# Kernel tuning notes

Hardware: AMD Instinct MI355X
Metric: run time of the kernel (lower is better)

## Reference

```python
import jax, jax.numpy as jnp
import numpy as np

DEV_VDW, VDW_N, MAXV, MINV, DM_MIN = 0.2, 6.0, 0.0356, 0.0178, 0.5


def setup_inputs() -> dict:
    key = jax.random.key(0)
    ks = iter(jax.random.split(key, 64))
    B, N1, N2, D, L = 8, 128, 256, 128, 3
    f = jnp.float32
    nrm = lambda shape, s=0.05: jax.random.normal(next(ks), shape, f) * s
    ligand_h = jax.random.normal(next(ks), (B, N1, 54), f)
    target_h = jax.random.normal(next(ks), (B, N2, 54), f)
    def adj(n):
        a = (jax.random.uniform(next(ks), (B, n, n)) < 0.08).astype(f)
        a = jnp.maximum(a, jnp.swapaxes(a, 1, 2))
        return jnp.maximum(a, jnp.eye(n, dtype=f))
    ligand_adj = adj(N1)
    target_adj = adj(N2)
    interaction_indice = jax.random.uniform(next(ks), (B, 3, N1, N2), f)
    ligand_pos = jax.random.normal(next(ks), (B, N1, 3), f) * 2.0
    target_pos = jax.random.normal(next(ks), (B, N2, 3), f) * 4.0
    rotor = jax.random.uniform(next(ks), (B,), f) * 10.0
    ligand_vdw_radii = 1.2 + 0.8 * jax.random.uniform(next(ks), (B, N1), f)
    target_vdw_radii = 1.2 + 0.8 * jax.random.uniform(next(ks), (B, N2), f)
    return dict(
        ligand_h=ligand_h, ligand_adj=ligand_adj, target_h=target_h, target_adj=target_adj,
        interaction_indice=interaction_indice, ligand_pos=ligand_pos, target_pos=target_pos,
        rotor=rotor, ligand_vdw_radii=ligand_vdw_radii, target_vdw_radii=target_vdw_radii,
        ligand_valid=jnp.ones((B, N1), f), target_valid=jnp.ones((B, N2), f),
        ligand_non_metal=jnp.ones((B, N1), f), target_non_metal=jnp.ones((B, N2), f),
        emb_w=nrm((54, D)),
        gat_w=nrm((L, D, D)), gat_b=jnp.zeros((L, D), f), gat_att=nrm((L, D, D)),
        gat_gate_w=nrm((L, 2 * D, 1)), gat_gate_b=jnp.zeros((L, 1), f),
        int_wt_w=nrm((L, D, D)), int_wt_b=jnp.zeros((L, D), f),
        int_mt_w=nrm((L, D, D)), int_mt_b=jnp.zeros((L, D), f),
        gru_w_ih=nrm((L, 3 * D, D)), gru_w_hh=nrm((L, 3 * D, D)),
        gru_b_ih=jnp.zeros((L, 3 * D), f), gru_b_hh=jnp.zeros((L, 3 * D), f),
        A_w1=nrm((2 * D, D)), A_b1=jnp.zeros((D,), f), A_w2=nrm((D, 1)), A_b2=jnp.zeros((1,), f),
        B_w1=nrm((2 * D, D)), B_b1=jnp.zeros((D,), f), B_w2=nrm((D, 1)), B_b2=jnp.zeros((1,), f),
        hbond_coeff=jnp.array([1.0], f), hydrophobic_coeff=jnp.array([0.5], f),
        rotor_coeff=jnp.array([0.5], f),
    )


def reference(ligand_h, ligand_adj, target_h, target_adj, interaction_indice, ligand_pos,
              target_pos, rotor, ligand_vdw_radii, target_vdw_radii, ligand_valid,
              target_valid, ligand_non_metal, target_non_metal, emb_w, gat_w, gat_b,
              gat_att, gat_gate_w, gat_gate_b, int_wt_w, int_wt_b, int_mt_w, int_mt_b,
              gru_w_ih, gru_w_hh, gru_b_ih, gru_b_hh, A_w1, A_b1, A_w2, A_b2, B_w1, B_b1,
              B_w2, B_b2, hbond_coeff, hydrophobic_coeff, rotor_coeff):
    B, D, L = ligand_h.shape[0], emb_w.shape[1], gat_w.shape[0]

    def dist(lpos):
        diff = lpos[:, :, None, :] - target_pos[:, None, :, :]
        dm = jnp.sqrt((diff * diff).sum(-1) + 1e-10)
        return jnp.where(dm < DM_MIN, 1e10, dm)

    dm = dist(ligand_pos)

    def gat(x, adj, i):
        nt = x @ gat_w[i] + gat_b[i]                                   # [B,N,D]
        ea = jnp.einsum('bjl,bkl->bjk', nt @ gat_att[i], nt)
        ea = ea + jnp.swapaxes(ea, 1, 2)
        aw = jax.nn.softmax(jnp.where(adj > 1e-6, ea, -9e15), axis=-1) * adj
        out = jax.nn.relu(jnp.einsum('bij,bjd->bid', aw, nt))
        gate = jax.nn.sigmoid(jnp.concatenate([x, out], -1) @ gat_gate_w[i] + gat_gate_b[i])
        return gate * x + (1.0 - gate) * out

    lh = ligand_h @ emb_w
    th = target_h @ emb_w
    for i in range(L):
        lh = gat(lh, ligand_adj, i)
        th = gat(th, target_adj, i)

    adj12 = jax.lax.stop_gradient(dm)
    adj12 = jnp.where(adj12 > 5.0, 0.0, adj12)
    adj12 = jnp.where(adj12 > 1e-3, 1.0, 0.0)
    adj21 = jnp.swapaxes(adj12, 1, 2)

    def inter(a1, a2, ev, i):
        t1 = a1 @ int_wt_w[i] + int_wt_b[i]
        m2 = a2 @ int_mt_w[i] + int_mt_b[i]                            # [B,N2,D]
        t2 = (m2[:, None, :, :] * ev[..., None]).max(axis=2)           # [B,N1,D]
        msg = jax.nn.relu(t1 + t2)
        gi = msg @ gru_w_ih[i].T + gru_b_ih[i]
        gh = a1 @ gru_w_hh[i].T + gru_b_hh[i]
        i_r, i_z, i_n = jnp.split(gi, 3, -1)
        h_r, h_z, h_n = jnp.split(gh, 3, -1)
        r = jax.nn.sigmoid(i_r + h_r)
        z = jax.nn.sigmoid(i_z + h_z)
        n = jnp.tanh(i_n + r * h_n)
        return (1.0 - z) * n + z * a1

    for i in range(L):
        lh, th = inter(lh, th, adj12, i), inter(th, lh, adj21, i)

    N1, N2 = lh.shape[1], th.shape[1]
    h_cat = jnp.concatenate([
        jnp.broadcast_to(lh[:, :, None, :], (B, N1, N2, D)),
        jnp.broadcast_to(th[:, None, :, :], (B, N1, N2, D))], -1)      # [B,N1,N2,2D]

    A_raw = jax.nn.sigmoid(jax.nn.relu(h_cat @ A_w1 + A_b1) @ A_w2 + A_b2)[..., 0]
    B_raw = jnp.tanh(jax.nn.relu(h_cat @ B_w1 + B_b1) @ B_w2 + B_b2)[..., 0] * DEV_VDW
    dm0 = ligand_vdw_radii[:, :, None] + target_vdw_radii[:, None, :] + B_raw
    valid_pair = ligand_non_metal[:, :, None] * target_non_metal[:, None, :]
    A_vdw = A_raw * (MAXV - MINV) + MINV

    def energies_of(dm):
        dm0c = jnp.where(dm0 < 1e-4, 1.0, dm0)
        r6 = (dm0c / dm) ** VDW_N
        evdw = A_vdw * (jnp.minimum(r6 * r6 - 2.0 * r6, 100.0) * valid_pair)
        vdw_val = evdw.sum((1, 2))[:, None]
        dmd = dm - dm0
        def hb(Aind):
            r = jnp.clip(dmd * Aind / -0.7, 0.0, 1.0) * -(hbond_coeff[0] * hbond_coeff[0])
            return r.sum((1, 2))[:, None]
        hbond = hb(interaction_indice[:, 0])
        metal = hb(interaction_indice[:, 1])
        hp = jnp.clip((-dmd + 1.5) * interaction_indice[:, 2], 0.0, 1.0)
        hp = hp * -(hydrophobic_coeff[0] * hydrophobic_coeff[0])
        e = jnp.concatenate([vdw_val, hbond, metal, hp.sum((1, 2))[:, None]], -1)
        return e / (1.0 + rotor_coeff[0] * rotor_coeff[0] * rotor[:, None])

    energies = energies_of(dm)
    esum = lambda p: energies_of(dist(p)).sum()
    g = jax.grad(esum)(ligand_pos)
    der1 = (g.sum(1) ** 2).mean()
    der2 = -jax.grad(lambda p: jax.grad(esum)(p).sum())(ligand_pos).sum((1, 2)).mean()
    return energies, der1, der2
```

## Files before the change

### kernel.cpp

```cpp
#include <hip/hip_runtime.h>
#include <math.h>

#define BB 8
#define N1C 128
#define N2C 256
#define DC 128
#define NHC 54
#define ROWS_L 1024
#define ROWS_T 2048
#define ROWS_ALL 3072

__device__ __forceinline__ float wredSum(float v) {
#pragma unroll
  for (int o = 32; o > 0; o >>= 1) v += __shfl_down(v, o);
  return v;
}
__device__ float blockSum(float v) {
  __shared__ float red[9];
  v = wredSum(v);
  int lane = threadIdx.x & 63, wid = threadIdx.x >> 6;
  __syncthreads();
  if (lane == 0) red[wid] = v;
  __syncthreads();
  if (threadIdx.x == 0) {
    float s = 0.f;
    int nw = (blockDim.x + 63) >> 6;
    for (int i = 0; i < nw; ++i) s += red[i];
    red[8] = s;
  }
  __syncthreads();
  return red[8];
}

__global__ __launch_bounds__(256) void k_prep(
    const float* __restrict__ LP, const float* __restrict__ TP,
    float* __restrict__ AD, const float* __restrict__ LH,
    const float* __restrict__ TH, const float* __restrict__ EW,
    float* __restrict__ H0, const float* __restrict__ GWp,
    const float* __restrict__ GBp, const float* __restrict__ ATT,
    float* __restrict__ WA, float* __restrict__ bA,
    const float* __restrict__ IH, const float* __restrict__ HH,
    float* __restrict__ GIHT, float* __restrict__ GHHT) {
  int bid = blockIdx.x, tid = threadIdx.x;
  if (bid < 1024) {
    long idx = (long)bid * 256 + tid;
    int j = idx & (N2C - 1);
    long t = idx >> 8;
    int i = (int)(t & (N1C - 1));
    int b = (int)(t >> 7);
    float dx = LP[((long)b * N1C + i) * 3 + 0] - TP[((long)b * N2C + j) * 3 + 0];
    float dy = LP[((long)b * N1C + i) * 3 + 1] - TP[((long)b * N2C + j) * 3 + 1];
    float dz = LP[((long)b * N1C + i) * 3 + 2] - TP[((long)b * N2C + j) * 3 + 2];
    float d = sqrtf(dx * dx + dy * dy + dz * dz + 1e-10f);
    if (d < 0.5f) d = 1e10f;
    AD[idx] = (d <= 5.0f && d > 1e-3f) ? 1.f : 0.f;
  } else if (bid < 1024 + 384) {
    int r0 = (bid - 1024) * 8;
    __shared__ float xs[8][NHC];
    for (int t = tid; t < 8 * NHC; t += 256) {
      int rr = r0 + t / NHC, c = t % NHC;
      xs[t / NHC][c] = (rr < ROWS_L) ? LH[(long)rr * NHC + c]
                                     : TH[(long)(rr - ROWS_L) * NHC + c];
    }
    __syncthreads();
    int d = tid & 127, rb = (tid >> 7) * 4;
    float a[4] = {0.f, 0.f, 0.f, 0.f};
#pragma unroll 6
    for (int k = 0; k < NHC; ++k) {
      float wv = EW[(long)k * DC + d];
#pragma unroll
      for (int r = 0; r < 4; ++r) a[r] += xs[rb + r][k] * wv;
    }
#pragma unroll
    for (int r = 0; r < 4; ++r) H0[(long)(r0 + rb + r) * DC + d] = a[r];
  } else if (bid < 1024 + 384 + 99) {
    int q = bid - 1408;
    int l = q / 33, bx = q % 33;
    const float* Wl = GWp + (long)l * DC * DC;
    const float* Al = ATT + (long)l * DC * DC;
    if (bx == 32) {
      if (tid < 128) {
        float acc = 0.f;
#pragma unroll 8
        for (int m = 0; m < DC; ++m)
          acc += GBp[l * DC + m] * Al[(long)m * DC + tid];
        bA[l * DC + tid] = acc;
      }
    } else {
      __shared__ float xs2[4][DC];
      int r0 = bx * 4;
      for (int t = tid; t < 4 * DC; t += 256)
        xs2[t >> 7][t & 127] = Wl[(long)r0 * DC + t];
      __syncthreads();
      if (tid < 128) {
        int d = tid;
        float a0 = 0.f, a1 = 0.f, a2 = 0.f, a3 = 0.f;
#pragma unroll 8
        for (int m = 0; m < DC; ++m) {
          float av = Al[(long)m * DC + d];
          a0 += xs2[0][m] * av;
          a1 += xs2[1][m] * av;
          a2 += xs2[2][m] * av;
          a3 += xs2[3][m] * av;
        }
        float* out = WA + (long)l * DC * DC + (long)r0 * DC + d;
        out[0] = a0;
        out[DC] = a1;
        out[2 * DC] = a2;
        out[3 * DC] = a3;
      }
    }
  } else {
    long idx = (long)(bid - 1507) * 256 + tid;
    if (idx < 6L * 49152) {
      int a = (int)(idx / 49152);
      int rem = (int)(idx % 49152);
      int l = a >> 1, whh = a & 1;
      int c = rem / 384, rr = rem % 384;
      const float* src = (whh ? HH : IH) + (long)l * 49152;
      float* dst = (whh ? GHHT : GIHT) + (long)l * 49152;
      dst[(long)c * 384 + rr] = src[(long)rr * 128 + c];
    }
  }
}

__global__ __launch_bounds__(256) void k_lin2h(
    const float* __restrict__ X, const float* __restrict__ W1,
    const float* __restrict__ b1, const float* __restrict__ W2,
    const float* __restrict__ b2, float* __restrict__ Y1,
    float* __restrict__ Y2) {
  int r0 = blockIdx.x * 4;
  __shared__ float xs_t[DC][4];
  int tid = threadIdx.x;
  for (int t = tid; t < 4 * DC; t += 256) {
    int r = t >> 7, c = t & 127;
    xs_t[c][r] = X[(long)(r0 + r) * DC + c];
  }
  __syncthreads();
  int h = tid >> 7, d = tid & 127;
  const float* W = h ? W2 : W1;
  const float* bp = h ? b2 : b1;
  float* Y = h ? Y2 : Y1;
  float a0 = 0.f, a1 = 0.f, a2 = 0.f, a3 = 0.f;
#pragma unroll 8
  for (int k = 0; k < DC; ++k) {
    float4 xv = *(const float4*)&xs_t[k][0];
    float wv = W[(long)k * DC + d];
    a0 = fmaf(xv.x, wv, a0);
    a1 = fmaf(xv.y, wv, a1);
    a2 = fmaf(xv.z, wv, a2);
    a3 = fmaf(xv.w, wv, a3);
  }
  float bv = bp ? bp[d] : 0.f;
  Y[(long)(r0 + 0) * DC + d] = a0 + bv;
  Y[(long)(r0 + 1) * DC + d] = a1 + bv;
  Y[(long)(r0 + 2) * DC + d] = a2 + bv;
  Y[(long)(r0 + 3) * DC + d] = a3 + bv;
}

__global__ __launch_bounds__(256) void k_featall(
    const float* __restrict__ X, const float* __restrict__ Aw1,
    const float* __restrict__ Ab1, const float* __restrict__ Bw1,
    const float* __restrict__ Bb1, float* __restrict__ UA,
    float* __restrict__ UB, float* __restrict__ VAT,
    float* __restrict__ VBT) {
  int bid = blockIdx.x;
  bool lig = bid < 256;
  int r0 = lig ? bid * 4 : ROWS_L + (bid - 256) * 4;
  __shared__ float xs_t[DC][4];
  int tid = threadIdx.x;
  for (int t = tid; t < 4 * DC; t += 256) {
    int r = t >> 7, c = t & 127;
    xs_t[c][r] = X[(long)(r0 + r) * DC + c];
  }
  __syncthreads();
  int h = tid >> 7, d = tid & 127;
  const float* W = (h ? Bw1 : Aw1) + (lig ? 0 : DC * DC);
  float a0 = 0.f, a1 = 0.f, a2 = 0.f, a3 = 0.f;
#pragma unroll 8
  for (int k = 0; k < DC; ++k) {
    float4 xv = *(const float4*)&xs_t[k][0];
    float wv = W[(long)k * DC + d];
    a0 = fmaf(xv.x, wv, a0);
    a1 = fmaf(xv.y, wv, a1);
    a2 = fmaf(xv.z, wv, a2);
    a3 = fmaf(xv.w, wv, a3);
  }
  if (lig) {
    float bv = h ? Bb1[d] : Ab1[d];
    float* Y = h ? UB : UA;
    Y[(long)(r0 + 0) * DC + d] = a0 + bv;
    Y[(long)(r0 + 1) * DC + d] = a1 + bv;
    Y[(long)(r0 + 2) * DC + d] = a2 + bv;
    Y[(long)(r0 + 3) * DC + d] = a3 + bv;
  } else {
    float* V = h ? VBT : VAT;
    int q = bid - 256;
    int b = q >> 6, rin = (q * 4) & 255;
    float* dst = &V[((long)b * DC + d) * N2C + rin];
    dst[0] = a0;
    dst[1] = a1;
    dst[2] = a2;
    dst[3] = a3;
  }
}

__global__ __launch_bounds__(256) void k_ea2(const float* __restrict__ NTp,
                                             const float* __restrict__ E1p,
                                             const float* __restrict__ ADJL,
                                             const float* __restrict__ ADJT,
                                             float* __restrict__ EAL,
                                             float* __restrict__ EAT) {
  int id = blockIdx.x;
  int N, base, j0, k0, b;
  const float* ADJ;
  float* EA;
  if (id < 64) {
    b = id >> 3;
    int rem = id & 7;
    N = N1C;
    base = b * N1C;
    j0 = (rem >> 1) * 32;
    k0 = (rem & 1) * 64;
    ADJ = ADJL + (long)b * N1C * N1C;
    EA = EAL + (long)b * N1C * N1C;
  } else {
    int q = id - 64;
    b = q >> 5;
    int rem = q & 31;
    N = N2C;
    base = ROWS_L + b * N2C;
    j0 = (rem >> 2) * 32;
    k0 = (rem & 3) * 64;
    ADJ = ADJT + (long)b * N2C * N2C;
    EA = EAT + (long)b * N2C * N2C;
  }
  __shared__ float aj_e1[32][34], aj_nt[32][34];
  __shared__ float bk_e1[32][68], bk_nt[32][68];
  int tid = threadIdx.x, tx = tid & 15, ty = tid >> 4;
  float acc[2][4];
#pragma unroll
  for (int r = 0; r < 2; ++r)
#pragma unroll
    for (int c = 0; c < 4; ++c) acc[r][c] = 0.f;
  for (int kc = 0; kc < DC; kc += 32) {
    __syncthreads();
    for (int t = tid; t < 1024; t += 256) {
      int kk = t & 31, rr = t >> 5;
      aj_e1[kk][rr] = E1p[(long)(base + j0 + rr) * DC + kc + kk];
      aj_nt[kk][rr] = NTp[(long)(base + j0 + rr) * DC + kc + kk];
    }
    for (int t = tid; t < 2048; t += 256) {
      int kk = t & 31, cc = t >> 5;
      bk_e1[kk][cc] = E1p[(long)(base + k0 + cc) * DC + kc + kk];
      bk_nt[kk][cc] = NTp[(long)(base + k0 + cc) * DC + kc + kk];
    }
    __syncthreads();
#pragma unroll
    for (int kk = 0; kk < 32; ++kk) {
      float2 ae = *(const float2*)&aj_e1[kk][ty * 2];
      float2 an = *(const float2*)&aj_nt[kk][ty * 2];
      float4 bn = *(const float4*)&bk_nt[kk][tx * 4];
      float4 be = *(const float4*)&bk_e1[kk][tx * 4];
      acc[0][0] = fmaf(ae.x, bn.x, fmaf(an.x, be.x, acc[0][0]));
      acc[0][1] = fmaf(ae.x, bn.y, fmaf(an.x, be.y, acc[0][1]));
      acc[0][2] = fmaf(ae.x, bn.z, fmaf(an.x, be.z, acc[0][2]));
      acc[0][3] = fmaf(ae.x, bn.w, fmaf(an.x, be.w, acc[0][3]));
      acc[1][0] = fmaf(ae.y, bn.x, fmaf(an.y, be.x, acc[1][0]));
      acc[1][1] = fmaf(ae.y, bn.y, fmaf(an.y, be.y, acc[1][1]));
      acc[1][2] = fmaf(ae.y, bn.z, fmaf(an.y, be.z, acc[1][2]));
      acc[1][3] = fmaf(ae.y, bn.w, fmaf(an.y, be.w, acc[1][3]));
    }
  }
#pragma unroll
  for (int r = 0; r < 2; ++r) {
    long rowi = (long)(j0 + ty * 2 + r) * N + k0 + tx * 4;
    float4 ad = *(const float4*)&ADJ[rowi];
    float4 o;
    o.x = (ad.x > 1e-6f) ? acc[r][0] : -9e15f;
    o.y = (ad.y > 1e-6f) ? acc[r][1] : -9e15f;
    o.z = (ad.z > 1e-6f) ? acc[r][2] : -9e15f;
    o.w = (ad.w > 1e-6f) ? acc[r][3] : -9e15f;
    *(float4*)&EA[rowi] = o;
  }
}

__global__ __launch_bounds__(512) void k_smagg3(
    const float* __restrict__ EAL, const float* __restrict__ EAT,
    const float* __restrict__ NTp, const float* __restrict__ Xp,
    const float* __restrict__ GW, const float* __restrict__ GB,
    float* __restrict__ Y) {
  int z = blockIdx.z;
  int N = z ? N2C : N1C;
  if (blockIdx.x * 16 >= N) return;
  int ls = z ? 8 : 7;
  int baseRow = z ? ROWS_L : 0;
  const float* EA = z ? EAT : EAL;
  int b = blockIdx.y, i0 = blockIdx.x * 16;
  __shared__ float ps[16][N2C + 4];
  __shared__ float col[32][DC + 4];
  __shared__ float red[16];
  int tid = threadIdx.x;
  const float* EAb = EA + (long)b * N * N + (long)i0 * N;
  for (int t = tid; t < 16 * N; t += 512)
    ps[t >> ls][t & (N - 1)] = EAb[t];
  __syncthreads();
  int r = tid >> 5, l = tid & 31;
  {
    float m = -INFINITY;
    for (int k = l; k < N; k += 32) m = fmaxf(m, ps[r][k]);
#pragma unroll
    for (int o = 16; o > 0; o >>= 1) m = fmaxf(m, __shfl_xor(m, o));
    float s = 0.f;
    for (int k = l; k < N; k += 32) {
      float p = expf(ps[r][k] - m);
      ps[r][k] = p;
      s += p;
    }
#pragma unroll
    for (int o = 16; o > 0; o >>= 1) s += __shfl_xor(s, o);
    float inv = 1.f / s;
    for (int k = l; k < N; k += 32) ps[r][k] *= inv;
  }
  int d0 = l * 4;
  float a0 = 0.f, a1 = 0.f, a2 = 0.f, a3 = 0.f;
  const float* NTb = NTp + (long)(baseRow + b * N) * DC;
  for (int k0 = 0; k0 < N; k0 += 32) {
    __syncthreads();
    for (int t = tid; t < 32 * DC; t += 512)
      col[t >> 7][t & 127] = NTb[(long)(k0 + (t >> 7)) * DC + (t & 127)];
    __syncthreads();
#pragma unroll 8
    for (int kk = 0; kk < 32; ++kk) {
      float4 c4 = *(const float4*)&col[kk][d0];
      float p = ps[r][k0 + kk];
      a0 = fmaf(p, c4.x, a0);
      a1 = fmaf(p, c4.y, a1);
      a2 = fmaf(p, c4.z, a2);
      a3 = fmaf(p, c4.w, a3);
    }
  }
  float4 gwd = *(const float4*)&GW[d0];
  float4 gwo = *(const float4*)&GW[DC + d0];
  float4 x4 = *(const float4*)&Xp[(long)(baseRow + b * N + i0 + r) * DC + d0];
  float o0 = fmaxf(a0, 0.f), o1 = fmaxf(a1, 0.f);
  float o2 = fmaxf(a2, 0.f), o3 = fmaxf(a3, 0.f);
  float part = x4.x * gwd.x + o0 * gwo.x + x4.y * gwd.y + o1 * gwo.y +
               x4.z * gwd.z + o2 * gwo.z + x4.w * gwd.w + o3 * gwo.w;
#pragma unroll
  for (int o = 16; o > 0; o >>= 1) part += __shfl_xor(part, o);
  if (l == 0) red[r] = part;
  __syncthreads();
  float g = 1.f / (1.f + expf(-(red[r] + GB[0])));
  float4 y;
  y.x = g * x4.x + (1.f - g) * o0;
  y.y = g * x4.y + (1.f - g) * o1;
  y.z = g * x4.z + (1.f - g) * o2;
  y.w = g * x4.w + (1.f - g) * o3;
  *(float4*)&Y[(long)(baseRow + b * N + i0 + r) * DC + d0] = y;
}

__global__ __launch_bounds__(512) void k_msggru(
    const float* __restrict__ T1, const float* __restrict__ M2,
    const float* __restrict__ EV, const float* __restrict__ Hp,
    const float* __restrict__ WihT, const float* __restrict__ WhhT,
    const float* __restrict__ bih, const float* __restrict__ bhh,
    float* __restrict__ Y) {
  int r0 = blockIdx.x * 4;
  __shared__ float m2s[32][DC + 4];
  __shared__ float evs[4][36];
  __shared__ float xs_t[DC][4], hs_t[DC][4];
  __shared__ float gis[4][384], ghs[4][384];
  int tid = threadIdx.x;
  int Nj, m2base, b, i0in;
  long ev_is, ev_js;
  if (r0 < ROWS_L) {
    b = r0 >> 7;
    i0in = r0 & 127;
    Nj = N2C;
    m2base = ROWS_L + b * N2C;
    ev_is = N2C;
    ev_js = 1;
  } else {
    int q = r0 - ROWS_L;
    b = q >> 8;
    i0in = q & 255;
    Nj = N1C;
    m2base = b * N1C;
    ev_is = 1;
    ev_js = N2C;
  }
  const float* EVb = EV + (long)b * (N1C * N2C);
  int r = tid >> 7, d = tid & 127;
  float acc = -INFINITY;
  for (int j0 = 0; j0 < Nj; j0 += 32) {
    __syncthreads();
    for (int t = tid; t < 32 * DC; t += 512)
      m2s[t >> 7][t & 127] = M2[(long)(m2base + j0 + (t >> 7)) * DC + (t & 127)];
    if (tid < 128)
      evs[tid >> 5][tid & 31] =
          EVb[(long)(i0in + (tid >> 5)) * ev_is + (long)(j0 + (tid & 31)) * ev_js];
    __syncthreads();
#pragma unroll 8
    for (int jj = 0; jj < 32; ++jj)
      acc = fmaxf(acc, m2s[jj][d] * evs[r][jj]);
  }
  xs_t[d][r] = fmaxf(T1[(long)(r0 + r) * DC + d] + acc, 0.f);
  for (int t = tid; t < 4 * DC; t += 512)
    hs_t[t & 127][t >> 7] = Hp[(long)(r0 + (t >> 7)) * DC + (t & 127)];
  __syncthreads();
  if (tid < 384) {
    int dd = tid;
    float ai[4] = {0.f, 0.f, 0.f, 0.f}, ah[4] = {0.f, 0.f, 0.f, 0.f};
#pragma unroll 8
    for (int k = 0; k < DC; ++k) {
      float4 xv = *(const float4*)&xs_t[k][0];
      float4 hv = *(const float4*)&hs_t[k][0];
      float wi = WihT[(long)k * 384 + dd];
      float wh = WhhT[(long)k * 384 + dd];
      ai[0] = fmaf(xv.x, wi, ai[0]);
      ai[1] = fmaf(xv.y, wi, ai[1]);
      ai[2] = fmaf(xv.z, wi, ai[2]);
      ai[3] = fmaf(xv.w, wi, ai[3]);
      ah[0] = fmaf(hv.x, wh, ah[0]);
      ah[1] = fmaf(hv.y, wh, ah[1]);
      ah[2] = fmaf(hv.z, wh, ah[2]);
      ah[3] = fmaf(hv.w, wh, ah[3]);
    }
    float bi = bih[dd], bh = bhh[dd];
#pragma unroll
    for (int rr = 0; rr < 4; ++rr) {
      gis[rr][dd] = ai[rr] + bi;
      ghs[rr][dd] = ah[rr] + bh;
    }
  }
  __syncthreads();
  for (int t = tid; t < 4 * DC; t += 512) {
    int rr = t >> 7, dq = t & 127;
    float ir = gis[rr][dq], iz = gis[rr][dq + 128], inn = gis[rr][dq + 256];
    float hr = ghs[rr][dq], hz = ghs[rr][dq + 128], hn = ghs[rr][dq + 256];
    float rg = 1.f / (1.f + expf(-(ir + hr)));
    float zg = 1.f / (1.f + expf(-(iz + hz)));
    float ng = tanhf(inn + rg * hn);
    Y[(long)(r0 + rr) * DC + dq] = (1.f - zg) * ng + zg * hs_t[dq][rr];
  }
}

__global__ __launch_bounds__(256) void k_pair(
    const float* __restrict__ UA, const float* __restrict__ VAT,
    const float* __restrict__ UB, const float* __restrict__ VBT,
    const float* __restrict__ AW2, const float* __restrict__ AB2,
    const float* __restrict__ BW2, const float* __restrict__ BB2,
    const float* __restrict__ LP, const float* __restrict__ TP,
    const float* __restrict__ LVDW, const float* __restrict__ TVDW,
    const float* __restrict__ LNM, const float* __restrict__ TNM,
    const float* __restrict__ II, const float* __restrict__ HBC,
    const float* __restrict__ HPC, float* __restrict__ PART) {
  const int D = DC, N1 = N1C, N2 = N2C;
  int i0 = blockIdx.x * 2, b = blockIdx.y, j = threadIdx.x;
  __shared__ float ua[2][128], ub[2][128], wa2[128], wb2[128];
  if (j < 128) {
    long rb = ((long)b * N1 + i0) * D + j;
    ua[0][j] = UA[rb];
    ub[0][j] = UB[rb];
    wa2[j] = AW2[j];
    wb2[j] = BW2[j];
  } else {
    int jj = j - 128;
    long rb = ((long)b * N1 + i0 + 1) * D + jj;
    ua[1][jj] = UA[rb];
    ub[1][jj] = UB[rb];
  }
  __syncthreads();
  const float* vat = VAT + (long)b * D * N2;
  const float* vbt = VBT + (long)b * D * N2;
  float dotA[2] = {0.f, 0.f}, dotB[2] = {0.f, 0.f};
#pragma unroll 4
  for (int d = 0; d < D; ++d) {
    float va = vat[(long)d * N2 + j];
    float vb = vbt[(long)d * N2 + j];
    dotA[0] += fmaxf(ua[0][d] + va, 0.f) * wa2[d];
    dotA[1] += fmaxf(ua[1][d] + va, 0.f) * wa2[d];
    dotB[0] += fmaxf(ub[0][d] + vb, 0.f) * wb2[d];
    dotB[1] += fmaxf(ub[1][d] + vb, 0.f) * wb2[d];
  }
  float hb2 = HBC[0] * HBC[0], hp2 = HPC[0] * HPC[0];
  float tx = TP[((long)b * N2 + j) * 3 + 0];
  float ty = TP[((long)b * N2 + j) * 3 + 1];
  float tz = TP[((long)b * N2 + j) * 3 + 2];
  float tvd = TVDW[b * N2 + j];
  float tnm = TNM[b * N2 + j];
  float res[2][8];
#pragma unroll
  for (int ii = 0; ii < 2; ++ii) {
    int i = i0 + ii;
    float A_raw = 1.f / (1.f + expf(-(dotA[ii] + AB2[0])));
    float A_vdw = A_raw * (0.0356f - 0.0178f) + 0.0178f;
    float B_raw = tanhf(dotB[ii] + BB2[0]) * 0.2f;

    float lx = LP[((long)b * N1 + i) * 3 + 0];
    float ly = LP[((long)b * N1 + i) * 3 + 1];
    float lz = LP[((long)b * N1 + i) * 3 + 2];
    float dx = lx - tx, dy = ly - ty, dz = lz - tz;
    float s2 = dx * dx + dy * dy + dz * dz + 1e-10f;
    float draw = sqrtf(s2);
    bool clamped = draw < 0.5f;
    float dmv = clamped ? 1e10f : draw;

    float dm0 = LVDW[b * N1 + i] + tvd + B_raw;
    float dm0c = (dm0 < 1e-4f) ? 1.f : dm0;
    float valid = LNM[b * N1 + i] * tnm;

    float rr = dm0c / dmv;
    float r2 = rr * rr, r6 = r2 * r2 * r2;
    float fv = r6 * r6 - 2.f * r6;
    float evdw = A_vdw * (fminf(fv, 100.f) * valid);

    float dmd = dmv - dm0;
    long ii0x = ((long)b * 3) * N1 * N2 + (long)i * N2 + j;
    float I0 = II[ii0x];
    float I1 = II[ii0x + (long)N1 * N2];
    float I2 = II[ii0x + 2L * N1 * N2];
    float u0 = dmd * I0 / (-0.7f);
    float u1 = dmd * I1 / (-0.7f);
    float vv = (1.5f - dmd) * I2;
    float ehb = fminf(fmaxf(u0, 0.f), 1.f) * (-hb2);
    float emt = fminf(fmaxf(u1, 0.f), 1.f) * (-hb2);
    float ehp = fminf(fmaxf(vv, 0.f), 1.f) * (-hp2);

    float gx = 0.f, gy = 0.f, gz = 0.f, d2t = 0.f;
    if (!clamped) {
      float Ep = 0.f, Epp = 0.f;
      if (fv < 100.f) {
        float c = A_vdw * valid;
        Ep += c * (-12.f) * r6 * (r6 - 1.f) / draw;
        Epp += c * r6 * (156.f * r6 - 84.f) / s2;
      }
      if (u0 > 0.f && u0 < 1.f) Ep += hb2 * I0 * (1.f / 0.7f);
      if (u1 > 0.f && u1 < 1.f) Ep += hb2 * I1 * (1.f / 0.7f);
      if (vv > 0.f && vv < 1.f) Ep += hp2 * I2;
      float invd = 1.f / draw;
      gx = Ep * dx * invd;
      gy = Ep * dy * invd;
      gz = Ep * dz * invd;
      float T = dx + dy + dz;
      float tt = T * T / s2;
      d2t = Epp * tt + Ep * (3.f - tt) * invd;
    }
    res[ii][0] = evdw;
    res[ii][1] = ehb;
    res[ii][2] = emt;
    res[ii][3] = ehp;
    res[ii][4] = gx;
    res[ii][5] = gy;
    res[ii][6] = gz;
    res[ii][7] = d2t;
  }
#pragma unroll
  for (int ii = 0; ii < 2; ++ii) {
    float o[8];
#pragma unroll
    for (int q = 0; q < 8; ++q) o[q] = blockSum(res[ii][q]);
    if (j == 0) {
      float* p = PART + ((long)b * N1 + i0 + ii) * 8;
#pragma unroll
      for (int q = 0; q < 8; ++q) p[q] = o[q];
    }
  }
}

__global__ void k_final(const float* __restrict__ PART, const float* __restrict__ ROT,
                        const float* __restrict__ RC, float* __restrict__ OUT) {
  const int N1 = N1C;
  __shared__ float s[8][8];
  int t = threadIdx.x;
  if (t < 64) {
    int b = t >> 3, k1 = t & 7;
    float acc = 0.f;
    for (int i = 0; i < N1; ++i) acc += PART[((long)b * N1 + i) * 8 + k1];
    s[b][k1] = acc;
  }
  __syncthreads();
  if (t == 0) {
    float rcc = RC[0] * RC[0];
    float der1 = 0.f, der2 = 0.f;
    for (int b = 0; b < 8; ++b) {
      float w = 1.f / (1.f + rcc * ROT[b]);
      OUT[b * 4 + 0] = s[b][0] * w;
      OUT[b * 4 + 1] = s[b][1] * w;
      OUT[b * 4 + 2] = s[b][2] * w;
      OUT[b * 4 + 3] = s[b][3] * w;
      for (int c = 0; c < 3; ++c) {
        float S = s[b][4 + c] * w;
        der1 += S * S;
      }
      der2 += s[b][7] * w;
    }
    OUT[32] = der1 / 24.f;
    OUT[33] = -der2 / 8.f;
  }
}

extern "C" void kernel_launch(void* const* d_in, const int* in_sizes, int n_in,
                              void* d_out, int out_size, void* d_ws, size_t ws_size,
                              hipStream_t stream) {
  (void)in_sizes; (void)n_in; (void)out_size; (void)ws_size;
  const int D = DC;

  const float* ligand_h   = (const float*)d_in[0];
  const float* ligand_adj = (const float*)d_in[1];
  const float* target_h   = (const float*)d_in[2];
  const float* target_adj = (const float*)d_in[3];
  const float* inter_ind  = (const float*)d_in[4];
  const float* ligand_pos = (const float*)d_in[5];
  const float* target_pos = (const float*)d_in[6];
  const float* rotor      = (const float*)d_in[7];
  const float* lvdw       = (const float*)d_in[8];
  const float* tvdw       = (const float*)d_in[9];
  const float* lnm        = (const float*)d_in[12];
  const float* tnm        = (const float*)d_in[13];
  const float* emb_w      = (const float*)d_in[14];
  const float* gat_w      = (const float*)d_in[15];
  const float* gat_b      = (const float*)d_in[16];
  const float* gat_att    = (const float*)d_in[17];
  const float* gat_gate_w = (const float*)d_in[18];
  const float* gat_gate_b = (const float*)d_in[19];
  const float* int_wt_w   = (const float*)d_in[20];
  const float* int_wt_b   = (const float*)d_in[21];
  const float* int_mt_w   = (const float*)d_in[22];
  const float* int_mt_b   = (const float*)d_in[23];
  const float* gru_w_ih   = (const float*)d_in[24];
  const float* gru_w_hh   = (const float*)d_in[25];
  const float* gru_b_ih   = (const float*)d_in[26];
  const float* gru_b_hh   = (const float*)d_in[27];
  const float* A_w1       = (const float*)d_in[28];
  const float* A_b1       = (const float*)d_in[29];
  const float* A_w2       = (const float*)d_in[30];
  const float* A_b2       = (const float*)d_in[31];
  const float* B_w1       = (const float*)d_in[32];
  const float* B_b1       = (const float*)d_in[33];
  const float* B_w2       = (const float*)d_in[34];
  const float* B_b2       = (const float*)d_in[35];
  const float* hb_c       = (const float*)d_in[36];
  const float* hp_c       = (const float*)d_in[37];
  const float* rc_c       = (const float*)d_in[38];

  float* w = (float*)d_ws;
  auto take = [&](size_t n) { float* p = w; w += n; return p; };
  float* H0    = take((size_t)ROWS_ALL * DC);
  float* H1    = take((size_t)ROWS_ALL * DC);
  float* NT    = take((size_t)ROWS_ALL * DC);
  float* E1    = take((size_t)ROWS_ALL * DC);
  float* EAL   = take((size_t)BB * N1C * N1C);
  float* EAT   = take((size_t)BB * N2C * N2C);
  float* ADJ12 = take((size_t)BB * N1C * N2C);
  float* WA    = take((size_t)3 * DC * DC);
  float* bA    = take((size_t)3 * DC);
  float* GIHT  = take((size_t)3 * DC * 384);
  float* GHHT  = take((size_t)3 * DC * 384);
  float* PART  = take((size_t)BB * N1C * 8);
  float* T1  = NT;
  float* M2  = E1;
  float* UA  = EAL;
  float* UB  = EAT;
  float* VAT = NT;
  float* VBT = E1;

  k_prep<<<2659, 256, 0, stream>>>(ligand_pos, target_pos, ADJ12, ligand_h,
                                   target_h, emb_w, H0, gat_w, gat_b, gat_att,
                                   WA, bA, gru_w_ih, gru_w_hh, GIHT, GHHT);

  float *cur = H0, *alt = H1;

  for (int l = 0; l < 3; ++l) {
    k_lin2h<<<ROWS_ALL / 4, 256, 0, stream>>>(
        cur, gat_w + (size_t)l * D * D, gat_b + l * D, WA + (size_t)l * D * D,
        bA + l * D, NT, E1);
    k_ea2<<<320, 256, 0, stream>>>(NT, E1, ligand_adj, target_adj, EAL, EAT);
    k_smagg3<<<dim3(N2C / 16, BB, 2), 512, 0, stream>>>(
        EAL, EAT, NT, cur, gat_gate_w + l * 2 * D, gat_gate_b + l, alt);
    float* t = cur; cur = alt; alt = t;
  }

  for (int l = 0; l < 3; ++l) {
    k_lin2h<<<ROWS_ALL / 4, 256, 0, stream>>>(
        cur, int_wt_w + (size_t)l * D * D, int_wt_b + l * D,
        int_mt_w + (size_t)l * D * D, int_mt_b + l * D, T1, M2);
    k_msggru<<<ROWS_ALL / 4, 512, 0, stream>>>(
        T1, M2, ADJ12, cur, GIHT + (size_t)l * D * 384,
        GHHT + (size_t)l * D * 384, gru_b_ih + l * 384, gru_b_hh + l * 384,
        alt);
    float* t = cur; cur = alt; alt = t;
  }

  k_featall<<<768, 256, 0, stream>>>(cur, A_w1, A_b1, B_w1, B_b1, UA, UB, VAT,
                                     VBT);

  k_pair<<<dim3(N1C / 2, BB), 256, 0, stream>>>(UA, VAT, UB, VBT, A_w2, A_b2,
                                                B_w2, B_b2, ligand_pos,
                                                target_pos, lvdw, tvdw, lnm,
                                                tnm, inter_ind, hb_c, hp_c,
                                                PART);

  k_final<<<1, 256, 0, stream>>>(PART, rotor, rc_c, (float*)d_out);
}
```

Baseline: 331.0 us.

## Process eight rows per block in message+GRU kernel to reuse M2 and weights

Each k_msggru block now handles 8 rows instead of 4, so every staged M2 tile and every GRU weight load from global memory serves twice as many rows. The max-aggregation keeps two accumulators per thread, and the GRU matmul runs in two passes of 4 rows. Shared memory is pooled so the gate buffers alias the M2/EV staging area, keeping the footprint in check. The cost is half as many blocks (384), which lowers parallelism on a GPU with many CUs.

```diff
diff --git a/kernel.cpp b/kernel.cpp
--- a/kernel.cpp
+++ b/kernel.cpp
@@ -366,18 +366,21 @@
     const float* __restrict__ WihT, const float* __restrict__ WhhT,
     const float* __restrict__ bih, const float* __restrict__ bhh,
     float* __restrict__ Y) {
-  int r0 = blockIdx.x * 4;
-  __shared__ float m2s[32][DC + 4];
-  __shared__ float evs[4][36];
-  __shared__ float xs_t[DC][4], hs_t[DC][4];
-  __shared__ float gis[4][384], ghs[4][384];
+  int r0 = blockIdx.x * 8;
+  __shared__ float pool[6144];
+  __shared__ float xs_t[DC][8], hs_t[DC][8];
+  float* m2s = pool;
+  float* evs = pool + 4224;
+  float* gis = pool;
+  float* ghs = pool + 3072;
   int tid = threadIdx.x;
-  int Nj, m2base, b, i0in;
+  int Nj, m2base, b, i0in, ntile;
   long ev_is, ev_js;
   if (r0 < ROWS_L) {
     b = r0 >> 7;
     i0in = r0 & 127;
     Nj = N2C;
+    ntile = N2C / 32;
     m2base = ROWS_L + b * N2C;
     ev_is = N2C;
     ev_js = 1;
@@ -386,59 +389,74 @@
     b = q >> 8;
     i0in = q & 255;
     Nj = N1C;
+    ntile = N1C / 32;
     m2base = b * N1C;
     ev_is = 1;
     ev_js = N2C;
   }
+  (void)Nj;
   const float* EVb = EV + (long)b * (N1C * N2C);
   int r = tid >> 7, d = tid & 127;
-  float acc = -INFINITY;
-  for (int j0 = 0; j0 < Nj; j0 += 32) {
+  float acc0 = -INFINITY, acc1 = -INFINITY;
+  for (int jt = 0; jt < ntile; ++jt) {
+    int j0 = jt * 32;
     __syncthreads();
     for (int t = tid; t < 32 * DC; t += 512)
-      m2s[t >> 7][t & 127] = M2[(long)(m2base + j0 + (t >> 7)) * DC + (t & 127)];
-    if (tid < 128)
-      evs[tid >> 5][tid & 31] =
-          EVb[(long)(i0in + (tid >> 5)) * ev_is + (long)(j0 + (tid & 31)) * ev_js];
+      m2s[(t >> 7) * 132 + (t & 127)] =
+          M2[(long)(m2base + j0 + (t >> 7)) * DC + (t & 127)];
+    if (tid < 256)
+      evs[(tid >> 5) * 36 + (tid & 31)] =
+          EVb[(long)(i0in + (tid >> 5)) * ev_is +
+              (long)(j0 + (tid & 31)) * ev_js];
     __syncthreads();
 #pragma unroll 8
-    for (int jj = 0; jj < 32; ++jj)
-      acc = fmaxf(acc, m2s[jj][d] * evs[r][jj]);
-  }
-  xs_t[d][r] = fmaxf(T1[(long)(r0 + r) * DC + d] + acc, 0.f);
-  for (int t = tid; t < 4 * DC; t += 512)
+    for (int jj = 0; jj < 32; ++jj) {
+      float m = m2s[jj * 132 + d];
+      acc0 = fmaxf(acc0, m * evs[r * 36 + jj]);
+      acc1 = fmaxf(acc1, m * evs[(r + 4) * 36 + jj]);
+    }
+  }
+  xs_t[d][r] = fmaxf(T1[(long)(r0 + r) * DC + d] + acc0, 0.f);
+  xs_t[d][r + 4] = fmaxf(T1[(long)(r0 + r + 4) * DC + d] + acc1, 0.f);
+  for (int t = tid; t < 8 * DC; t += 512)
     hs_t[t & 127][t >> 7] = Hp[(long)(r0 + (t >> 7)) * DC + (t & 127)];
   __syncthreads();
   if (tid < 384) {
     int dd = tid;
-    float ai[4] = {0.f, 0.f, 0.f, 0.f}, ah[4] = {0.f, 0.f, 0.f, 0.f};
+    float bi = bih[dd], bh = bhh[dd];
+#pragma unroll 1
+    for (int pass = 0; pass < 2; ++pass) {
+      int rb = pass * 4;
+      float ai[4] = {0.f, 0.f, 0.f, 0.f}, ah[4] = {0.f, 0.f, 0.f, 0.f};
 #pragma unroll 8
-    for (int k = 0; k < DC; ++k) {
-      float4 xv = *(const float4*)&xs_t[k][0];
-      float4 hv = *(const float4*)&hs_t[k][0];
-      float wi = WihT[(long)k * 384 + dd];
-      float wh = WhhT[(long)k * 384 + dd];
-      ai[0] = fmaf(xv.x, wi, ai[0]);
-      ai[1] = fmaf(xv.y, wi, ai[1]);
-      ai[2] = fmaf(xv.z, wi, ai[2]);
-      ai[3] = fmaf(xv.w, wi, ai[3]);
-      ah[0] = fmaf(hv.x, wh, ah[0]);
-      ah[1] = fmaf(hv.y, wh, ah[1]);
-      ah[2] = fmaf(hv.z, wh, ah[2]);
-      ah[3] = fmaf(hv.w, wh, ah[3]);
-    }
-    float bi = bih[dd], bh = bhh[dd];
-#pragma unroll
-    for (int rr = 0; rr < 4; ++rr) {
-      gis[rr][dd] = ai[rr] + bi;
-      ghs[rr][dd] = ah[rr] + bh;
-    }
-  }
-  __syncthreads();
-  for (int t = tid; t < 4 * DC; t += 512) {
+      for (int k = 0; k < DC; ++k) {
+        float4 xv = *(const float4*)&xs_t[k][rb];
+        float4 hv = *(const float4*)&hs_t[k][rb];
+        float wi = WihT[(long)k * 384 + dd];
+        float wh = WhhT[(long)k * 384 + dd];
+        ai[0] = fmaf(xv.x, wi, ai[0]);
+        ai[1] = fmaf(xv.y, wi, ai[1]);
+        ai[2] = fmaf(xv.z, wi, ai[2]);
+        ai[3] = fmaf(xv.w, wi, ai[3]);
+        ah[0] = fmaf(hv.x, wh, ah[0]);
+        ah[1] = fmaf(hv.y, wh, ah[1]);
+        ah[2] = fmaf(hv.z, wh, ah[2]);
+        ah[3] = fmaf(hv.w, wh, ah[3]);
+      }
+#pragma unroll
+      for (int rr = 0; rr < 4; ++rr) {
+        gis[(rb + rr) * 384 + dd] = ai[rr] + bi;
+        ghs[(rb + rr) * 384 + dd] = ah[rr] + bh;
+      }
+    }
+  }
+  __syncthreads();
+  for (int t = tid; t < 8 * DC; t += 512) {
     int rr = t >> 7, dq = t & 127;
-    float ir = gis[rr][dq], iz = gis[rr][dq + 128], inn = gis[rr][dq + 256];
-    float hr = ghs[rr][dq], hz = ghs[rr][dq + 128], hn = ghs[rr][dq + 256];
+    float ir = gis[rr * 384 + dq], iz = gis[rr * 384 + dq + 128],
+          inn = gis[rr * 384 + dq + 256];
+    float hr = ghs[rr * 384 + dq], hz = ghs[rr * 384 + dq + 128],
+          hn = ghs[rr * 384 + dq + 256];
     float rg = 1.f / (1.f + expf(-(ir + hr)));
     float zg = 1.f / (1.f + expf(-(iz + hz)));
     float ng = tanhf(inn + rg * hn);
@@ -686,7 +704,7 @@
     k_lin2h<<<ROWS_ALL / 4, 256, 0, stream>>>(
         cur, int_wt_w + (size_t)l * D * D, int_wt_b + l * D,
         int_mt_w + (size_t)l * D * D, int_mt_b + l * D, T1, M2);
-    k_msggru<<<ROWS_ALL / 4, 512, 0, stream>>>(
+    k_msggru<<<ROWS_ALL / 8, 512, 0, stream>>>(
         T1, M2, ADJ12, cur, GIHT + (size_t)l * D * 384,
         GHHT + (size_t)l * D * 384, gru_b_ih + l * 384, gru_b_hh + l * 384,
         alt);
```

Result: faster. 310.0 us (-6.3%).
